# Performance work log

Hardware: AMD Instinct MI355X
Metric: run time of the kernel (lower is better)

## Reference

```python
import jax, jax.numpy as jnp
import numpy as np

B, C, H, W = 1, 64, 64, 64


def conv3x3(x, w, b):
    y = jax.lax.conv_general_dilated(x, w, (1, 1), [(1, 1), (1, 1)],
                                     dimension_numbers=('NCHW', 'OIHW', 'NCHW'))
    return y + b[None, :, None, None]


def deform_conv(x, offset, w, b, pad, dil):
    # torchvision-style DeformConv2d, 1 deformable group, stride 1, 3x3 kernel.
    Bn, Cn, Hn, Wn = x.shape
    Co, Ci, kh, kw = w.shape
    K = kh * kw
    off = offset.reshape(Bn, K, 2, Hn, Wn)  # (dy, dx) per kernel tap
    ky, kx = jnp.meshgrid(jnp.arange(kh), jnp.arange(kw), indexing='ij')
    ky = (ky.reshape(K) * dil).astype(x.dtype)
    kx = (kx.reshape(K) * dil).astype(x.dtype)
    py = (jnp.arange(Hn, dtype=x.dtype) - pad)[None, None, :, None] + ky[None, :, None, None] + off[:, :, 0]
    px = (jnp.arange(Wn, dtype=x.dtype) - pad)[None, None, None, :] + kx[None, :, None, None] + off[:, :, 1]
    y0 = jnp.floor(py)
    x0 = jnp.floor(px)
    xf = x.reshape(Bn, Cn, Hn * Wn)

    def gather(yi, xi):
        valid = ((yi >= 0) & (yi <= Hn - 1) & (xi >= 0) & (xi <= Wn - 1)).astype(x.dtype)
        idx = jnp.clip(yi, 0, Hn - 1) * Wn + jnp.clip(xi, 0, Wn - 1)
        v = jax.vmap(lambda xb, ib: jnp.take(xb, ib, axis=1))(xf, idx.reshape(Bn, -1))
        return v.reshape(Bn, Cn, K, Hn, Wn), valid

    y0i = y0.astype(jnp.int32)
    x0i = x0.astype(jnp.int32)
    v00, m00 = gather(y0i, x0i)
    v01, m01 = gather(y0i, x0i + 1)
    v10, m10 = gather(y0i + 1, x0i)
    v11, m11 = gather(y0i + 1, x0i + 1)
    wy = py - y0
    wx = px - x0
    w00 = (1 - wy) * (1 - wx) * m00
    w01 = (1 - wy) * wx * m01
    w10 = wy * (1 - wx) * m10
    w11 = wy * wx * m11
    sampled = (v00 * w00[:, None] + v01 * w01[:, None] +
               v10 * w10[:, None] + v11 * w11[:, None])  # [B,C,K,H,W]
    return jnp.einsum('bckhw,ock->bohw', sampled, w.reshape(Co, Ci, K)) + b[None, :, None, None]


def resize(x, h, w):
    # matches F.interpolate(mode='bilinear', align_corners=False)
    return jax.image.resize(x, (x.shape[0], x.shape[1], h, w), method='bilinear')


def setup_inputs() -> dict:
    key = jax.random.key(0)
    ks = jax.random.split(key, 9)
    s = 1.0 / np.sqrt(C * 9)
    inp = {'x': jax.random.normal(ks[0], (B, C, H, W), jnp.float32)}
    for i in range(4):
        inp[f'w_off{i}'] = jax.random.normal(ks[1 + i], (18, C, 3, 3), jnp.float32) * s
        inp[f'b_off{i}'] = jnp.zeros((18,), jnp.float32)
        inp[f'w_c{i}'] = jax.random.normal(ks[5 + i], (C // 4, C, 3, 3), jnp.float32) * s
        inp[f'b_c{i}'] = jnp.zeros((C // 4,), jnp.float32)
    return inp


def reference(x, w_off0, b_off0, w_off1, b_off1, w_off2, b_off2, w_off3, b_off3,
              w_c0, b_c0, w_c1, b_c1, w_c2, b_c2, w_c3, b_c3):
    leaky = lambda t: jax.nn.leaky_relu(t, 0.01)
    gelu = lambda t: jax.nn.gelu(t, approximate=False)
    Hh, Ww = x.shape[2], x.shape[3]
    x_1 = resize(x, Hh // 2, Ww // 2)
    x_2 = resize(x, 2 * Hh, 2 * Ww)
    x_3 = resize(x_2, 4 * Hh, 4 * Ww)
    off1 = conv3x3(x_1, w_off0, b_off0)
    off0 = conv3x3(x, w_off1, b_off1)
    off2 = conv3x3(x_2, w_off2, b_off2)
    off3 = conv3x3(x_3, w_off3, b_off3)
    a1 = leaky(deform_conv(x_1, off1, w_c3, b_c3, pad=4, dil=4))
    a = leaky(deform_conv(x, off0, w_c2, b_c2, pad=3, dil=3))
    a2 = leaky(deform_conv(x_2, off2, w_c1, b_c1, pad=2, dil=2))
    a3 = leaky(deform_conv(x_3, off3, w_c0, b_c0, pad=1, dil=1))
    x1 = resize(a1, Hh, Ww)
    x2 = resize(a2, Hh, Ww)
    x3 = resize(a3, Hh, Ww)
    l = gelu(x1)
    m = gelu(a - l)
    h = gelu(x2 - a)
    s = gelu(x3 - x2)
    return (l, m, h, s)
```

## Files before the change

kernel.cpp:

```cpp
#include <hip/hip_runtime.h>
#include <math.h>

#define BDIM 256

typedef float v2f __attribute__((ext_vector_type(2)));

__device__ __forceinline__ v2f pkfma(v2f a, v2f b, v2f c) {
#if __has_builtin(__builtin_elementwise_fma)
  return __builtin_elementwise_fma(a, b, c);
#else
  v2f d;
  d.x = fmaf(a.x, b.x, c.x);
  d.y = fmaf(a.y, b.y, c.y);
  return d;
#endif
}

__device__ __forceinline__ int resize_taps(int out_n, int o, int in_n,
                                           float* w, int* i0) {
  float inv_scale = (float)in_n / (float)out_n;
  float ks = inv_scale > 1.f ? inv_scale : 1.f;
  float sf = ((float)o + 0.5f) * inv_scale - 0.5f;
  int lo = (int)ceilf(sf - ks);
  int hi = (int)floorf(sf + ks);
  if (lo < 0) lo = 0;
  if (hi > in_n - 1) hi = in_n - 1;
  int n = hi - lo + 1;
  float sum = 0.f;
  for (int k = 0; k < n; ++k) {
    float t = 1.f - fabsf((float)(lo + k) - sf) / ks;
    t = t > 0.f ? t : 0.f;
    w[k] = t;
    sum += t;
  }
  float inv = 1.f / sum;
  for (int k = 0; k < n; ++k) w[k] *= inv;
  *i0 = lo;
  return n;
}

__device__ __forceinline__ float resize_one(const float* __restrict__ plane,
                                            int Hi, int Wi, int oy, int ox,
                                            int Ho, int Wo) {
  float wy[8], wx[8];
  int y0, x0;
  int ny = resize_taps(Ho, oy, Hi, wy, &y0);
  int nx = resize_taps(Wo, ox, Wi, wx, &x0);
  float acc = 0.f;
  for (int a = 0; a < ny; ++a) {
    const float* row = plane + (y0 + a) * Wi + x0;
    float r = 0.f;
    for (int b = 0; b < nx; ++b) r += wx[b] * row[b];
    acc += wy[a] * r;
  }
  return acc;
}

__device__ __forceinline__ void up2(int o, int n, int* t, float* w) {
  int m = o >> 1;
  if (o == 0) { t[0] = 0; w[0] = 1.f; t[1] = 0; w[1] = 0.f; }
  else if (o == 2 * n - 1) { t[0] = n - 1; w[0] = 1.f; t[1] = n - 1; w[1] = 0.f; }
  else if (o & 1) { t[0] = m; w[0] = 0.75f; t[1] = m + 1; w[1] = 0.25f; }
  else { t[0] = m - 1; w[0] = 0.25f; t[1] = m; w[1] = 0.75f; }
}

__global__ void k_front(const float* __restrict__ x, float* __restrict__ x1s,
                        float* __restrict__ x2s, float* __restrict__ x3s,
                        const float* __restrict__ d0, const float* __restrict__ d1,
                        const float* __restrict__ d2, const float* __restrict__ d3,
                        const float* __restrict__ c0, const float* __restrict__ c1,
                        const float* __restrict__ c2, const float* __restrict__ c3,
                        float* __restrict__ wT) {
  int idx = blockIdx.x * BDIM + threadIdx.x;
  if (idx < 65536) {
    int ox = idx & 31, oy = (idx >> 5) & 31, c = idx >> 10;
    x1s[idx] = resize_one(x + c * 4096, 64, 64, oy, ox, 32, 32);
  } else if (idx < 1114112) {
    int j = idx - 65536;
    int ox = j & 127, oy = (j >> 7) & 127, c = j >> 14;
    x2s[j] = resize_one(x + c * 4096, 64, 64, oy, ox, 128, 128);
  } else if (idx < 5308416) {
    int j = idx - 1114112;
    int ox = j & 255, oy = (j >> 8) & 255, c = j >> 16;
    int ty[2], tx[2];
    float twy[2], twx[2];
    up2(oy, 128, ty, twy);
    up2(ox, 128, tx, twx);
    int ry[4], rx[4];
    float rwy[4], rwx[4];
#pragma unroll
    for (int a = 0; a < 2; ++a) {
      int t2[2];
      float w2[2];
      up2(ty[a], 64, t2, w2);
      ry[2 * a] = t2[0]; rwy[2 * a] = twy[a] * w2[0];
      ry[2 * a + 1] = t2[1]; rwy[2 * a + 1] = twy[a] * w2[1];
      up2(tx[a], 64, t2, w2);
      rx[2 * a] = t2[0]; rwx[2 * a] = twx[a] * w2[0];
      rx[2 * a + 1] = t2[1]; rwx[2 * a + 1] = twx[a] * w2[1];
    }
    const float* xc = x + c * 4096;
    float acc = 0.f;
#pragma unroll
    for (int a = 0; a < 4; ++a) {
      const float* row = xc + ry[a] * 64;
      float r = 0.f;
#pragma unroll
      for (int b = 0; b < 4; ++b) r += rwx[b] * row[rx[b]];
      acc += rwy[a] * r;
    }
    x3s[j] = acc;
  } else if (idx < 5386752) {
    int w = idx - 5308416;
    if (w < 36864) {
      int i = w / 9216, r = w % 9216;
      int o = r % 16, t = r / 16, c = t % 64, k = t / 64;
      const float* s = i == 0 ? d0 : i == 1 ? d1 : i == 2 ? d2 : d3;
      wT[w] = s[(o * 64 + c) * 9 + k];
    } else {
      int j = w - 36864;
      int i = j / 10368, r = j % 10368;
      int o = r % 18, t = r / 18, c = t % 64, k = t / 64;
      const float* s = i == 0 ? c0 : i == 1 ? c1 : i == 2 ? c2 : c3;
      wT[w] = s[(o * 64 + c) * 9 + k];
    }
  }
}

struct FArgs {
  const float* in[4];
  const float* wc[4];
  const float* bc[4];
  const float* wd[4];
  const float* bd[4];
  float* out[4];
};

__global__ __launch_bounds__(512, 4) void k_fused(FArgs A) {
  __shared__ float red[8 * 64 * 18];
  int b = blockIdx.x;
  int s, b0, nseg;
  if (b < 1024)      { s = 3; b0 = 0;    nseg = 1024; }
  else if (b < 1280) { s = 2; b0 = 1024; nseg = 256; }
  else if (b < 1344) { s = 1; b0 = 1280; nseg = 64; }
  else               { s = 0; b0 = 1344; nseg = 16; }
  int bl = b - b0;
  int swz = (bl & 7) * (nseg >> 3) + (bl >> 3);
  int H = 32 << s, W = H, lw = 5 + s, HW = H * W;
  int pad = 4 - s, dil = pad;
  const float* in = A.in[s];
  int tid = threadIdx.x, lane = tid & 63;
  int gv = tid >> 6;
  int g = __builtin_amdgcn_readfirstlane(gv);
  int p = swz * 64 + lane;
  int py = p >> lw, px = p & (W - 1);
  const float* ipg = in + (size_t)(g * 8) * HW;
  float* myred = &red[(size_t)(gv * 64 + lane) * 18];
  const float* lred = &red[lane * 18];

  {
    v2f accA[9];
#pragma unroll
    for (int j = 0; j < 9; ++j) accA[j] = (v2f){0.f, 0.f};
    const float* wT = A.wc[s];
#pragma unroll
    for (int ky = 0; ky < 3; ++ky) {
#pragma unroll
      for (int kx = 0; kx < 3; ++kx) {
        int k = ky * 3 + kx;
        int yy = py + ky - 1, xx = px + kx - 1;
        float msk = (yy >= 0 && yy < H && xx >= 0 && xx < W) ? 1.f : 0.f;
        int ai = min(max(yy, 0), H - 1) * W + min(max(xx, 0), W - 1);
        float va[8];
        {
          const float* ip = ipg + ai;
#pragma unroll
          for (int c = 0; c < 8; ++c, ip += HW) va[c] = *ip;
        }
        const v2f* wk2 = (const v2f*)(wT + (size_t)(k * 64 + g * 8) * 18);
#pragma unroll
        for (int c = 0; c < 8; ++c, wk2 += 9) {
          float v = va[c] * msk;
          v2f vv = {v, v};
#pragma unroll
          for (int j = 0; j < 9; ++j) accA[j] = pkfma(wk2[j], vv, accA[j]);
        }
      }
    }
#pragma unroll
    for (int j = 0; j < 9; ++j) *(v2f*)(myred + 2 * j) = accA[j];
  }
  __syncthreads();
  v2f off2[9];
  {
    const v2f* bc2 = (const v2f*)A.bc[s];
#pragma unroll
    for (int j = 0; j < 9; ++j) {
      v2f v = bc2[j];
#pragma unroll
      for (int r = 0; r < 8; ++r) v += *(const v2f*)(lred + (size_t)r * 64 * 18 + 2 * j);
      off2[j] = v;
    }
  }
  __syncthreads();

  v2f acc2[8];
#pragma unroll
  for (int j = 0; j < 8; ++j) acc2[j] = (v2f){0.f, 0.f};
  {
    const float* wT = A.wd[s];
#pragma unroll
    for (int ky = 0; ky < 3; ++ky) {
#pragma unroll
      for (int kx = 0; kx < 3; ++kx) {
        int k = ky * 3 + kx;
        float dy = off2[k].x;
        float dx = off2[k].y;
        float pyf = (float)(py - pad + ky * dil) + dy;
        float pxf = (float)(px - pad + kx * dil) + dx;
        float fy0 = floorf(pyf), fx0 = floorf(pxf);
        float wy = pyf - fy0, wxv = pxf - fx0;
        int y0 = (int)fy0, x0 = (int)fx0;
        float xg = (x0 >= -1 && x0 <= W - 1) ? 1.f : 0.f;
        float r0 = (1.f - wy) * ((y0 >= 0 && y0 < H) ? xg : 0.f);
        float r1 = wy * ((y0 + 1 >= 0 && y0 + 1 < H) ? xg : 0.f);
        float cl = 1.f - wxv, cr = wxv;
        bool xlo = x0 < 0, xhi = x0 > W - 2;
        float W00 = xlo ? r0 * cr : (xhi ? 0.f : r0 * cl);
        float W01 = xlo ? 0.f : (xhi ? r0 * cl : r0 * cr);
        float W10 = xlo ? r1 * cr : (xhi ? 0.f : r1 * cl);
        float W11 = xlo ? 0.f : (xhi ? r1 * cl : r1 * cr);
        int ax = min(max(x0, 0), W - 2);
        int cy0 = min(max(y0, 0), H - 1);
        int cy1 = min(max(y0 + 1, 0), H - 1);
        int A0 = cy0 * W + ax, A1 = cy1 * W + ax;
        float v00[8], v01[8], v10[8], v11[8];
        {
          const float* ip = ipg;
#pragma unroll
          for (int c = 0; c < 8; ++c, ip += HW) {
            v00[c] = ip[A0];
            v01[c] = ip[A0 + 1];
            v10[c] = ip[A1];
            v11[c] = ip[A1 + 1];
          }
        }
        const v2f* wk2 = (const v2f*)(wT + (size_t)(k * 64 + g * 8) * 16);
#pragma unroll
        for (int c = 0; c < 8; ++c, wk2 += 8) {
          float sv = W00 * v00[c] + W01 * v01[c] + W10 * v10[c] + W11 * v11[c];
          v2f vv = {sv, sv};
#pragma unroll
          for (int j = 0; j < 8; ++j) acc2[j] = pkfma(wk2[j], vv, acc2[j]);
        }
      }
    }
  }
  if (gv) {
    float* wr = &red[(size_t)((gv - 1) * 64 + lane) * 18];
#pragma unroll
    for (int j = 0; j < 8; ++j) *(v2f*)(wr + 2 * j) = acc2[j];
  }
  __syncthreads();
  if (!gv) {
    const v2f* bd2 = (const v2f*)A.bd[s];
    float* out = A.out[s];
#pragma unroll
    for (int j = 0; j < 8; ++j) {
      v2f v = acc2[j] + bd2[j];
#pragma unroll
      for (int r = 0; r < 7; ++r) v += *(const v2f*)(lred + (size_t)r * 64 * 18 + 2 * j);
      float vx = v.x, vy = v.y;
      vx = vx >= 0.f ? vx : 0.01f * vx;
      vy = vy >= 0.f ? vy : 0.01f * vy;
      out[(size_t)(2 * j) * HW + p] = vx;
      out[(size_t)(2 * j + 1) * HW + p] = vy;
    }
  }
}

__global__ void k_hpass(const float* __restrict__ a2, const float* __restrict__ a3,
                        float* __restrict__ t2, float* __restrict__ t3) {
  int idx = blockIdx.x * BDIM + threadIdx.x;
  if (idx < 262144) {
    int ox = idx & 63, y = (idx >> 6) & 255, c = idx >> 14;
    float wx[8];
    int x0;
    int n = resize_taps(64, ox, 256, wx, &x0);
    const float* row = a3 + (size_t)c * 65536 + y * 256 + x0;
    float r = 0.f;
    for (int b = 0; b < n; ++b) r += wx[b] * row[b];
    t3[idx] = r;
  } else {
    int j = idx - 262144;
    if (j < 131072) {
      int ox = j & 63, y = (j >> 6) & 127, c = j >> 13;
      float wx[8];
      int x0;
      int n = resize_taps(64, ox, 128, wx, &x0);
      const float* row = a2 + (size_t)c * 16384 + y * 128 + x0;
      float r = 0.f;
      for (int b = 0; b < n; ++b) r += wx[b] * row[b];
      t2[j] = r;
    }
  }
}

__device__ __forceinline__ float gelu_f(float x) {
  return 0.5f * x * (1.f + erff(x * 0.70710678118654752f));
}

__global__ void k_final2(const float* __restrict__ a0, const float* __restrict__ a1,
                         const float* __restrict__ t2, const float* __restrict__ t3,
                         float* __restrict__ out) {
  int i = blockIdx.x * BDIM + threadIdx.x;
  int x = i & 63, y = (i >> 6) & 63, c = i >> 12;
  float x1r = resize_one(a1 + c * 1024, 32, 32, y, x, 64, 64);
  float wv[8];
  int y0;
  int n2 = resize_taps(64, y, 128, wv, &y0);
  const float* tp2 = t2 + (size_t)c * 8192 + y0 * 64 + x;
  float x2r = 0.f;
  for (int a = 0; a < n2; ++a) x2r += wv[a] * tp2[a * 64];
  int n3 = resize_taps(64, y, 256, wv, &y0);
  const float* tp3 = t3 + (size_t)c * 16384 + y0 * 64 + x;
  float x3r = 0.f;
  for (int a = 0; a < n3; ++a) x3r += wv[a] * tp3[a * 64];
  float av = a0[i];
  float l = gelu_f(x1r);
  float m = gelu_f(av - l);
  float h = gelu_f(x2r - av);
  float sv = gelu_f(x3r - x2r);
  out[i] = l;
  out[65536 + i] = m;
  out[131072 + i] = h;
  out[196608 + i] = sv;
}

static inline int cdiv(int a, int b) { return (a + b - 1) / b; }

extern "C" void kernel_launch(void* const* d_in, const int* in_sizes, int n_in,
                              void* d_out, int out_size, void* d_ws, size_t ws_size,
                              hipStream_t stream) {
  (void)in_sizes; (void)n_in; (void)out_size; (void)ws_size;
  const float* x = (const float*)d_in[0];
  const float* w_off[4] = {(const float*)d_in[1], (const float*)d_in[5],
                           (const float*)d_in[9], (const float*)d_in[13]};
  const float* b_off[4] = {(const float*)d_in[2], (const float*)d_in[6],
                           (const float*)d_in[10], (const float*)d_in[14]};
  const float* w_c[4] = {(const float*)d_in[3], (const float*)d_in[7],
                         (const float*)d_in[11], (const float*)d_in[15]};
  const float* b_c[4] = {(const float*)d_in[4], (const float*)d_in[8],
                         (const float*)d_in[12], (const float*)d_in[16]};
  float* out = (float*)d_out;

  float* ws = (float*)d_ws;
  float* a0 = ws;
  float* a1 = ws + 65536;
  float* a2 = ws + 81920;
  float* wT = ws + 344064;
  float* x1s = ws + 422400;
  float* t3 = ws + 422400;
  float* t2 = ws + 684544;
  float* x2s = ws + 875008;
  float* x3s = ws + 1923584;
  float* a3 = ws + 6117888;
  float* wTd = wT;
  float* wTc = wT + 36864;

  FArgs fa;
  const float* ins[4] = {x1s, x, x2s, x3s};
  float* as[4] = {a1, a0, a2, a3};
  for (int s = 0; s < 4; ++s) {
    fa.in[s] = ins[s];
    fa.wc[s] = wTc + s * 10368;
    fa.bc[s] = b_off[s];
    fa.wd[s] = wTd + (3 - s) * 9216;
    fa.bd[s] = b_c[3 - s];
    fa.out[s] = as[s];
  }

  k_front<<<cdiv(5386752, BDIM), BDIM, 0, stream>>>(
      x, x1s, x2s, x3s, w_c[0], w_c[1], w_c[2], w_c[3],
      w_off[0], w_off[1], w_off[2], w_off[3], wT);
  k_fused<<<1360, 512, 0, stream>>>(fa);
  k_hpass<<<cdiv(262144 + 131072, BDIM), BDIM, 0, stream>>>(a2, a3, t2, t3);
  k_final2<<<cdiv(65536, BDIM), BDIM, 0, stream>>>(a0, a1, t2, t3, out);
}
```

Before: 198.4 us.

## Store resized inputs channel-pair interleaved for 64-bit gathers in fused deform conv

The front kernel now writes all four scale inputs, including a new copy of x, in a layout that interleaves channel pairs per pixel. The fused kernel loads float2 per pixel instead of two separate scalar loads. It also does the bilinear blend with packed FMAs on channel pairs. This halves the number of gather instructions in the offset conv and the deformable sampling, at the cost of writing an extra packed copy of x and making the front-kernel stores strided.

New measurement: 180.1 us. -9.2%, faster.

```diff
diff --git a/kernel.cpp b/kernel.cpp
--- a/kernel.cpp
+++ b/kernel.cpp
@@ -64,8 +64,14 @@
   else { t[0] = m - 1; w[0] = 0.25f; t[1] = m; w[1] = 0.75f; }
 }
 
-__global__ void k_front(const float* __restrict__ x, float* __restrict__ x1s,
-                        float* __restrict__ x2s, float* __restrict__ x3s,
+__device__ __forceinline__ void pstore(float* __restrict__ dst, int c, int pix,
+                                       int HW, float v) {
+  dst[((size_t)(c >> 1) * HW + pix) * 2 + (c & 1)] = v;
+}
+
+__global__ void k_front(const float* __restrict__ x, float* __restrict__ x1p,
+                        float* __restrict__ x2p, float* __restrict__ x3p,
+                        float* __restrict__ xp,
                         const float* __restrict__ d0, const float* __restrict__ d1,
                         const float* __restrict__ d2, const float* __restrict__ d3,
                         const float* __restrict__ c0, const float* __restrict__ c1,
@@ -74,11 +80,13 @@
   int idx = blockIdx.x * BDIM + threadIdx.x;
   if (idx < 65536) {
     int ox = idx & 31, oy = (idx >> 5) & 31, c = idx >> 10;
-    x1s[idx] = resize_one(x + c * 4096, 64, 64, oy, ox, 32, 32);
+    pstore(x1p, c, oy * 32 + ox, 1024,
+           resize_one(x + c * 4096, 64, 64, oy, ox, 32, 32));
   } else if (idx < 1114112) {
     int j = idx - 65536;
     int ox = j & 127, oy = (j >> 7) & 127, c = j >> 14;
-    x2s[j] = resize_one(x + c * 4096, 64, 64, oy, ox, 128, 128);
+    pstore(x2p, c, oy * 128 + ox, 16384,
+           resize_one(x + c * 4096, 64, 64, oy, ox, 128, 128));
   } else if (idx < 5308416) {
     int j = idx - 1114112;
     int ox = j & 255, oy = (j >> 8) & 255, c = j >> 16;
@@ -109,7 +117,7 @@
       for (int b = 0; b < 4; ++b) r += rwx[b] * row[rx[b]];
       acc += rwy[a] * r;
     }
-    x3s[j] = acc;
+    pstore(x3p, c, oy * 256 + ox, 65536, acc);
   } else if (idx < 5386752) {
     int w = idx - 5308416;
     if (w < 36864) {
@@ -124,6 +132,10 @@
       const float* s = i == 0 ? c0 : i == 1 ? c1 : i == 2 ? c2 : c3;
       wT[w] = s[(o * 64 + c) * 9 + k];
     }
+  } else if (idx < 5648896) {
+    int j = idx - 5386752;
+    int c = j >> 12, pix = j & 4095;
+    pstore(xp, c, pix, 4096, x[j]);
   }
 }
 
@@ -148,13 +160,12 @@
   int swz = (bl & 7) * (nseg >> 3) + (bl >> 3);
   int H = 32 << s, W = H, lw = 5 + s, HW = H * W;
   int pad = 4 - s, dil = pad;
-  const float* in = A.in[s];
   int tid = threadIdx.x, lane = tid & 63;
   int gv = tid >> 6;
   int g = __builtin_amdgcn_readfirstlane(gv);
   int p = swz * 64 + lane;
   int py = p >> lw, px = p & (W - 1);
-  const float* ipg = in + (size_t)(g * 8) * HW;
+  const v2f* ipg2 = (const v2f*)A.in[s] + (size_t)(g * 4) * HW;
   float* myred = &red[(size_t)(gv * 64 + lane) * 18];
   const float* lred = &red[lane * 18];
 
@@ -171,19 +182,21 @@
         int yy = py + ky - 1, xx = px + kx - 1;
         float msk = (yy >= 0 && yy < H && xx >= 0 && xx < W) ? 1.f : 0.f;
         int ai = min(max(yy, 0), H - 1) * W + min(max(xx, 0), W - 1);
-        float va[8];
-        {
-          const float* ip = ipg + ai;
-#pragma unroll
-          for (int c = 0; c < 8; ++c, ip += HW) va[c] = *ip;
-        }
-        const v2f* wk2 = (const v2f*)(wT + (size_t)(k * 64 + g * 8) * 18);
-#pragma unroll
-        for (int c = 0; c < 8; ++c, wk2 += 9) {
-          float v = va[c] * msk;
-          v2f vv = {v, v};
-#pragma unroll
-          for (int j = 0; j < 9; ++j) accA[j] = pkfma(wk2[j], vv, accA[j]);
+        v2f va[4];
+#pragma unroll
+        for (int cp = 0; cp < 4; ++cp) va[cp] = ipg2[(size_t)cp * HW + ai];
+        const float* wkb = wT + (size_t)(k * 64 + g * 8) * 18;
+#pragma unroll
+        for (int cp = 0; cp < 4; ++cp) {
+          float vx = va[cp].x * msk;
+          float vy = va[cp].y * msk;
+          const v2f* w0 = (const v2f*)(wkb + (2 * cp) * 18);
+          const v2f* w1 = (const v2f*)(wkb + (2 * cp + 1) * 18);
+          v2f vvx = {vx, vx}, vvy = {vy, vy};
+#pragma unroll
+          for (int j = 0; j < 9; ++j) accA[j] = pkfma(w0[j], vvx, accA[j]);
+#pragma unroll
+          for (int j = 0; j < 9; ++j) accA[j] = pkfma(w1[j], vvy, accA[j]);
         }
       }
     }
@@ -234,24 +247,31 @@
         int cy0 = min(max(y0, 0), H - 1);
         int cy1 = min(max(y0 + 1, 0), H - 1);
         int A0 = cy0 * W + ax, A1 = cy1 * W + ax;
-        float v00[8], v01[8], v10[8], v11[8];
-        {
-          const float* ip = ipg;
-#pragma unroll
-          for (int c = 0; c < 8; ++c, ip += HW) {
-            v00[c] = ip[A0];
-            v01[c] = ip[A0 + 1];
-            v10[c] = ip[A1];
-            v11[c] = ip[A1 + 1];
-          }
+        v2f W00v = {W00, W00}, W01v = {W01, W01};
+        v2f W10v = {W10, W10}, W11v = {W11, W11};
+        v2f q00[4], q01[4], q10[4], q11[4];
+#pragma unroll
+        for (int cp = 0; cp < 4; ++cp) {
+          const v2f* ipp = ipg2 + (size_t)cp * HW;
+          q00[cp] = ipp[A0];
+          q01[cp] = ipp[A0 + 1];
+          q10[cp] = ipp[A1];
+          q11[cp] = ipp[A1 + 1];
         }
-        const v2f* wk2 = (const v2f*)(wT + (size_t)(k * 64 + g * 8) * 16);
-#pragma unroll
-        for (int c = 0; c < 8; ++c, wk2 += 8) {
-          float sv = W00 * v00[c] + W01 * v01[c] + W10 * v10[c] + W11 * v11[c];
-          v2f vv = {sv, sv};
-#pragma unroll
-          for (int j = 0; j < 8; ++j) acc2[j] = pkfma(wk2[j], vv, acc2[j]);
+        const float* wkb = wT + (size_t)(k * 64 + g * 8) * 16;
+#pragma unroll
+        for (int cp = 0; cp < 4; ++cp) {
+          v2f sv2 = q00[cp] * W00v;
+          sv2 = pkfma(q01[cp], W01v, sv2);
+          sv2 = pkfma(q10[cp], W10v, sv2);
+          sv2 = pkfma(q11[cp], W11v, sv2);
+          const v2f* w0 = (const v2f*)(wkb + (2 * cp) * 16);
+          const v2f* w1 = (const v2f*)(wkb + (2 * cp + 1) * 16);
+          v2f vvx = {sv2.x, sv2.x}, vvy = {sv2.y, sv2.y};
+#pragma unroll
+          for (int j = 0; j < 8; ++j) acc2[j] = pkfma(w0[j], vvx, acc2[j]);
+#pragma unroll
+          for (int j = 0; j < 8; ++j) acc2[j] = pkfma(w1[j], vvy, acc2[j]);
         }
       }
     }
@@ -359,17 +379,18 @@
   float* a1 = ws + 65536;
   float* a2 = ws + 81920;
   float* wT = ws + 344064;
-  float* x1s = ws + 422400;
+  float* x1p = ws + 422400;
   float* t3 = ws + 422400;
   float* t2 = ws + 684544;
-  float* x2s = ws + 875008;
-  float* x3s = ws + 1923584;
+  float* x2p = ws + 875008;
+  float* x3p = ws + 1923584;
   float* a3 = ws + 6117888;
+  float* xp = ws + 7166464;
   float* wTd = wT;
   float* wTc = wT + 36864;
 
   FArgs fa;
-  const float* ins[4] = {x1s, x, x2s, x3s};
+  const float* ins[4] = {x1p, xp, x2p, x3p};
   float* as[4] = {a1, a0, a2, a3};
   for (int s = 0; s < 4; ++s) {
     fa.in[s] = ins[s];
@@ -380,8 +401,8 @@
     fa.out[s] = as[s];
   }
 
-  k_front<<<cdiv(5386752, BDIM), BDIM, 0, stream>>>(
-      x, x1s, x2s, x3s, w_c[0], w_c[1], w_c[2], w_c[3],
+  k_front<<<cdiv(5648896, BDIM), BDIM, 0, stream>>>(
+      x, x1p, x2p, x3p, xp, w_c[0], w_c[1], w_c[2], w_c[3],
       w_off[0], w_off[1], w_off[2], w_off[3], wT);
   k_fused<<<1360, 512, 0, stream>>>(fa);
   k_hpass<<<cdiv(262144 + 131072, BDIM), BDIM, 0, stream>>>(a2, a3, t2, t3);
```

## Store resized inputs in channel-quad interleaved layout for vectorized gathers

Applied to the files above, without the earlier changes.

The front kernel now writes the resized inputs (and a copy of x) in a layout where groups of 4 channels are interleaved per pixel. The fused offset-conv and deformable-conv kernel can then fetch 4 channels with one 16-byte load instead of 4 strided scalar loads. The bilinear blend is done with 4-wide FMAs. This is meant to cut the number of gather instructions and improve cache-line use. The cost is strided scalar stores in the front kernel and an extra pass that rewrites x.

New measurement: 179.4 us. 9.6% less time.

```diff
diff --git a/kernel.cpp b/kernel.cpp
--- a/kernel.cpp
+++ b/kernel.cpp
@@ -4,6 +4,7 @@
 #define BDIM 256
 
 typedef float v2f __attribute__((ext_vector_type(2)));
+typedef float v4f __attribute__((ext_vector_type(4)));
 
 __device__ __forceinline__ v2f pkfma(v2f a, v2f b, v2f c) {
 #if __has_builtin(__builtin_elementwise_fma)
@@ -12,6 +13,19 @@
   v2f d;
   d.x = fmaf(a.x, b.x, c.x);
   d.y = fmaf(a.y, b.y, c.y);
+  return d;
+#endif
+}
+
+__device__ __forceinline__ v4f pkfma4(v4f a, v4f b, v4f c) {
+#if __has_builtin(__builtin_elementwise_fma)
+  return __builtin_elementwise_fma(a, b, c);
+#else
+  v4f d;
+  d.x = fmaf(a.x, b.x, c.x);
+  d.y = fmaf(a.y, b.y, c.y);
+  d.z = fmaf(a.z, b.z, c.z);
+  d.w = fmaf(a.w, b.w, c.w);
   return d;
 #endif
 }
@@ -64,8 +78,14 @@
   else { t[0] = m - 1; w[0] = 0.25f; t[1] = m; w[1] = 0.75f; }
 }
 
-__global__ void k_front(const float* __restrict__ x, float* __restrict__ x1s,
-                        float* __restrict__ x2s, float* __restrict__ x3s,
+__device__ __forceinline__ void pstore4(float* __restrict__ dst, int c, int pix,
+                                        int HW, float v) {
+  dst[((size_t)(c >> 2) * HW + pix) * 4 + (c & 3)] = v;
+}
+
+__global__ void k_front(const float* __restrict__ x, float* __restrict__ x1q,
+                        float* __restrict__ x2q, float* __restrict__ x3q,
+                        float* __restrict__ xq,
                         const float* __restrict__ d0, const float* __restrict__ d1,
                         const float* __restrict__ d2, const float* __restrict__ d3,
                         const float* __restrict__ c0, const float* __restrict__ c1,
@@ -74,11 +94,13 @@
   int idx = blockIdx.x * BDIM + threadIdx.x;
   if (idx < 65536) {
     int ox = idx & 31, oy = (idx >> 5) & 31, c = idx >> 10;
-    x1s[idx] = resize_one(x + c * 4096, 64, 64, oy, ox, 32, 32);
+    pstore4(x1q, c, oy * 32 + ox, 1024,
+            resize_one(x + c * 4096, 64, 64, oy, ox, 32, 32));
   } else if (idx < 1114112) {
     int j = idx - 65536;
     int ox = j & 127, oy = (j >> 7) & 127, c = j >> 14;
-    x2s[j] = resize_one(x + c * 4096, 64, 64, oy, ox, 128, 128);
+    pstore4(x2q, c, oy * 128 + ox, 16384,
+            resize_one(x + c * 4096, 64, 64, oy, ox, 128, 128));
   } else if (idx < 5308416) {
     int j = idx - 1114112;
     int ox = j & 255, oy = (j >> 8) & 255, c = j >> 16;
@@ -109,7 +131,7 @@
       for (int b = 0; b < 4; ++b) r += rwx[b] * row[rx[b]];
       acc += rwy[a] * r;
     }
-    x3s[j] = acc;
+    pstore4(x3q, c, oy * 256 + ox, 65536, acc);
   } else if (idx < 5386752) {
     int w = idx - 5308416;
     if (w < 36864) {
@@ -124,6 +146,10 @@
       const float* s = i == 0 ? c0 : i == 1 ? c1 : i == 2 ? c2 : c3;
       wT[w] = s[(o * 64 + c) * 9 + k];
     }
+  } else if (idx < 5648896) {
+    int j = idx - 5386752;
+    int c = j >> 12, pix = j & 4095;
+    pstore4(xq, c, pix, 4096, x[j]);
   }
 }
 
@@ -148,13 +174,12 @@
   int swz = (bl & 7) * (nseg >> 3) + (bl >> 3);
   int H = 32 << s, W = H, lw = 5 + s, HW = H * W;
   int pad = 4 - s, dil = pad;
-  const float* in = A.in[s];
   int tid = threadIdx.x, lane = tid & 63;
   int gv = tid >> 6;
   int g = __builtin_amdgcn_readfirstlane(gv);
   int p = swz * 64 + lane;
   int py = p >> lw, px = p & (W - 1);
-  const float* ipg = in + (size_t)(g * 8) * HW;
+  const v4f* ipg4 = (const v4f*)A.in[s] + (size_t)(g * 2) * HW;
   float* myred = &red[(size_t)(gv * 64 + lane) * 18];
   const float* lred = &red[lane * 18];
 
@@ -171,19 +196,24 @@
         int yy = py + ky - 1, xx = px + kx - 1;
         float msk = (yy >= 0 && yy < H && xx >= 0 && xx < W) ? 1.f : 0.f;
         int ai = min(max(yy, 0), H - 1) * W + min(max(xx, 0), W - 1);
-        float va[8];
-        {
-          const float* ip = ipg + ai;
-#pragma unroll
-          for (int c = 0; c < 8; ++c, ip += HW) va[c] = *ip;
+        v4f va0 = ipg4[ai];
+        v4f va1 = ipg4[(size_t)HW + ai];
+        const float* wkb = wT + (size_t)(k * 64 + g * 8) * 18;
+#pragma unroll
+        for (int e = 0; e < 4; ++e) {
+          float v = va0[e] * msk;
+          const v2f* w0 = (const v2f*)(wkb + e * 18);
+          v2f vv = {v, v};
+#pragma unroll
+          for (int j = 0; j < 9; ++j) accA[j] = pkfma(w0[j], vv, accA[j]);
         }
-        const v2f* wk2 = (const v2f*)(wT + (size_t)(k * 64 + g * 8) * 18);
-#pragma unroll
-        for (int c = 0; c < 8; ++c, wk2 += 9) {
-          float v = va[c] * msk;
+#pragma unroll
+        for (int e = 0; e < 4; ++e) {
+          float v = va1[e] * msk;
+          const v2f* w1 = (const v2f*)(wkb + (4 + e) * 18);
           v2f vv = {v, v};
 #pragma unroll
-          for (int j = 0; j < 9; ++j) accA[j] = pkfma(wk2[j], vv, accA[j]);
+          for (int j = 0; j < 9; ++j) accA[j] = pkfma(w1[j], vv, accA[j]);
         }
       }
     }
@@ -234,24 +264,39 @@
         int cy0 = min(max(y0, 0), H - 1);
         int cy1 = min(max(y0 + 1, 0), H - 1);
         int A0 = cy0 * W + ax, A1 = cy1 * W + ax;
-        float v00[8], v01[8], v10[8], v11[8];
+        v4f W00v = {W00, W00, W00, W00}, W01v = {W01, W01, W01, W01};
+        v4f W10v = {W10, W10, W10, W10}, W11v = {W11, W11, W11, W11};
+        const float* wkb = wT + (size_t)(k * 64 + g * 8) * 16;
         {
-          const float* ip = ipg;
-#pragma unroll
-          for (int c = 0; c < 8; ++c, ip += HW) {
-            v00[c] = ip[A0];
-            v01[c] = ip[A0 + 1];
-            v10[c] = ip[A1];
-            v11[c] = ip[A1 + 1];
+          v4f q00 = ipg4[A0], q01 = ipg4[A0 + 1];
+          v4f q10 = ipg4[A1], q11 = ipg4[A1 + 1];
+          v4f sv = q00 * W00v;
+          sv = pkfma4(q01, W01v, sv);
+          sv = pkfma4(q10, W10v, sv);
+          sv = pkfma4(q11, W11v, sv);
+#pragma unroll
+          for (int e = 0; e < 4; ++e) {
+            const v2f* w0 = (const v2f*)(wkb + e * 16);
+            v2f vv = {sv[e], sv[e]};
+#pragma unroll
+            for (int j = 0; j < 8; ++j) acc2[j] = pkfma(w0[j], vv, acc2[j]);
           }
         }
-        const v2f* wk2 = (const v2f*)(wT + (size_t)(k * 64 + g * 8) * 16);
-#pragma unroll
-        for (int c = 0; c < 8; ++c, wk2 += 8) {
-          float sv = W00 * v00[c] + W01 * v01[c] + W10 * v10[c] + W11 * v11[c];
-          v2f vv = {sv, sv};
-#pragma unroll
-          for (int j = 0; j < 8; ++j) acc2[j] = pkfma(wk2[j], vv, acc2[j]);
+        {
+          const v4f* ipq = ipg4 + (size_t)HW;
+          v4f q00 = ipq[A0], q01 = ipq[A0 + 1];
+          v4f q10 = ipq[A1], q11 = ipq[A1 + 1];
+          v4f sv = q00 * W00v;
+          sv = pkfma4(q01, W01v, sv);
+          sv = pkfma4(q10, W10v, sv);
+          sv = pkfma4(q11, W11v, sv);
+#pragma unroll
+          for (int e = 0; e < 4; ++e) {
+            const v2f* w1 = (const v2f*)(wkb + (4 + e) * 16);
+            v2f vv = {sv[e], sv[e]};
+#pragma unroll
+            for (int j = 0; j < 8; ++j) acc2[j] = pkfma(w1[j], vv, acc2[j]);
+          }
         }
       }
     }
@@ -359,17 +404,18 @@
   float* a1 = ws + 65536;
   float* a2 = ws + 81920;
   float* wT = ws + 344064;
-  float* x1s = ws + 422400;
+  float* x1q = ws + 422400;
   float* t3 = ws + 422400;
   float* t2 = ws + 684544;
-  float* x2s = ws + 875008;
-  float* x3s = ws + 1923584;
+  float* x2q = ws + 875008;
+  float* x3q = ws + 1923584;
   float* a3 = ws + 6117888;
+  float* xq = ws + 7166464;
   float* wTd = wT;
   float* wTc = wT + 36864;
 
   FArgs fa;
-  const float* ins[4] = {x1s, x, x2s, x3s};
+  const float* ins[4] = {x1q, xq, x2q, x3q};
   float* as[4] = {a1, a0, a2, a3};
   for (int s = 0; s < 4; ++s) {
     fa.in[s] = ins[s];
@@ -380,8 +426,8 @@
     fa.out[s] = as[s];
   }
 
-  k_front<<<cdiv(5386752, BDIM), BDIM, 0, stream>>>(
-      x, x1s, x2s, x3s, w_c[0], w_c[1], w_c[2], w_c[3],
+  k_front<<<cdiv(5648896, BDIM), BDIM, 0, stream>>>(
+      x, x1q, x2q, x3q, xq, w_c[0], w_c[1], w_c[2], w_c[3],
       w_off[0], w_off[1], w_off[2], w_off[3], wT);
   k_fused<<<1360, 512, 0, stream>>>(fa);
   k_hpass<<<cdiv(262144 + 131072, BDIM), BDIM, 0, stream>>>(a2, a3, t2, t3);
```
